# Kernel tuning notes

Hardware: AMD Instinct MI355X
Metric: run time of the kernel (lower is better)

The kernel has to match this reference:

```python
import math
import jax, jax.numpy as jnp
import numpy as np

B, N, D = 16, 2048, 256
EPS = 1e-8  # torch cosine_similarity default eps
TAU = 3.0   # gumbel-softmax temperature


def setup_inputs() -> dict:
    key = jax.random.key(0)
    k1, k2 = jax.random.split(key)
    return {
        "LowLevelFeatures": jax.random.normal(k1, (B, 1, N, D), dtype=jnp.float32),
        "HighLevelFeatures": jax.random.normal(k2, (B, 1, N, D), dtype=jnp.float32),
        "batch_size": B,
    }


def _forward(LLF4, HLF4):
    LLF = LLF4[:, 0]  # [B,N,D]
    HLF = HLF4[:, 0]  # [B,N,D]
    b, n, d = LLF.shape
    # pairwise cosine similarity [B,N,N]: matmul + norm-product (same math as
    # torch's broadcast cosine_similarity, without the [B,N,N,D] intermediate)
    dots = jnp.einsum('bnd,bmd->bnm', LLF, HLF)
    nl = jnp.linalg.norm(LLF, axis=-1)  # [B,N]
    nh = jnp.linalg.norm(HLF, axis=-1)  # [B,N]
    sim = dots / jnp.maximum(nl[:, :, None] * nh[:, None, :], EPS)
    sim = sim / math.sqrt(d)
    probs = jax.nn.softmax(sim, axis=1)  # softmax over dim 1 (LLF rows)
    # F.gumbel_softmax(probs, tau=3, hard=True, dim=1): probs act as logits
    u = jax.random.uniform(jax.random.key(42), probs.shape,
                           minval=1e-10, maxval=1.0)
    gumbels = -jnp.log(-jnp.log(u))
    y_soft = jax.nn.softmax((probs + gumbels) / TAU, axis=1)
    idx = jnp.argmax(y_soft, axis=1)  # [B,N]: selected LLF-row n per HLF col m
    # torch.where on the one-hot scans row-major over (b, n, m), so per batch
    # the returned n-indices are the SORTED multiset of selected indices
    sl = jnp.sort(idx, axis=-1)  # [B,N]
    bidx = jnp.arange(b)[:, None]  # [B,1]
    aligned = HLF[bidx, sl]  # gather along dim 1 -> [B,N,D]
    # rowwise cosine similarity between gathered HLF and LLF
    w = jnp.sum(aligned * LLF, axis=-1) / jnp.maximum(
        jnp.linalg.norm(aligned, axis=-1) * nl, EPS)  # [B,N]
    noise = jax.nn.softmax(w / 0.1, axis=1)[:, :, None]  # [B,N,1]
    hlf_new = aligned + LLF * noise
    out = HLF.at[bidx, sl].set(hlf_new)
    return out


def reference(LowLevelFeatures, HighLevelFeatures, batch_size):
    return _forward(LowLevelFeatures, HighLevelFeatures)
```

## Files before the change

kernel.cpp:

```cpp
#include <hip/hip_runtime.h>
#include <math.h>

#define NB 16
#define NN 2048
#define ND 256
#define BNtot (NB*NN)
#define HH 33554432u

typedef __attribute__((ext_vector_type(8))) short bf16x8;
typedef __attribute__((ext_vector_type(4))) float f32x4;

__device__ __forceinline__ void gld16(const void* g, void* l){
  __builtin_amdgcn_global_load_lds((const __attribute__((address_space(1))) void*)g,
                                   (__attribute__((address_space(3))) void*)l, 16, 0, 0);
}

__device__ __forceinline__ unsigned rotl(unsigned v, int r){
  return __builtin_amdgcn_alignbit(v, v, 32-r);
}
__device__ __forceinline__ unsigned umaxu(unsigned a, unsigned b){ return a > b ? a : b; }
__device__ __forceinline__ unsigned uminu(unsigned a, unsigned b){ return a < b ? a : b; }

__device__ __forceinline__ float gumbelv(unsigned b, unsigned n, unsigned m){
  unsigned f = (b<<22) | (n<<11) | m;
  unsigned x0 = (b < 8u) ? f : (f - HH);
  unsigned x1 = x0 + HH;
  const unsigned ks0=0u, ks1=42u, ks2=0u^42u^0x1BD11BDAu;
  unsigned v0 = x0 + ks0;
  unsigned v1 = x1 + ks1;
#define TFR(r) { v0 += v1; v1 = rotl(v1,(r)); v1 ^= v0; }
  TFR(13) TFR(15) TFR(26) TFR(6)
  v0 += ks1; v1 += ks2 + 1u;
  TFR(17) TFR(29) TFR(16) TFR(24)
  v0 += ks2; v1 += ks0 + 2u;
  TFR(13) TFR(15) TFR(26) TFR(6)
  v0 += ks0; v1 += ks1 + 3u;
  TFR(17) TFR(29) TFR(16) TFR(24)
  v0 += ks1; v1 += ks2 + 4u;
  TFR(13) TFR(15) TFR(26) TFR(6)
  v0 += ks2; v1 += ks0 + 5u;
#undef TFR
  unsigned bits = (b < 8u) ? v0 : v1;
  float fl = __uint_as_float((bits>>9) | 0x3F800000u) - 1.0f;
  float u = fmaxf(1e-10f, fl + 1e-10f);
  return -logf(-logf(u));
}

__device__ __forceinline__ float gfromkey(unsigned key){
  float fl = __uint_as_float(key | 0x3F800000u) - 1.0f;
  float u = fmaxf(1e-10f, fl + 1e-10f);
  return -logf(-logf(u));
}

__global__ void knorms(const float* __restrict__ LLF, const float* __restrict__ HLF,
                       float* __restrict__ nl, float* __restrict__ nh){
  int row = blockIdx.x;
  int wave = threadIdx.x >> 6;
  int lane = threadIdx.x & 63;
  const float* src = wave ? HLF : LLF;
  float4 v = ((const float4*)(src + (size_t)row*ND))[lane];
  float s = v.x*v.x + v.y*v.y + v.z*v.z + v.w*v.w;
  for (int o=32;o;o>>=1) s += __shfl_down(s,o);
  if (lane==0) (wave? nh: nl)[row] = sqrtf(s);
}

__launch_bounds__(256)
__global__ void kprep(const float* __restrict__ LLF, const float* __restrict__ HLF,
                      ushort* __restrict__ Abf, ushort* __restrict__ Bbf,
                      float* __restrict__ nl, float* __restrict__ nh){
  int w    = threadIdx.x >> 6;
  int lane = threadIdx.x & 63;
  int r = blockIdx.x*4 + w;
  const float* src = blockIdx.y ? HLF : LLF;
  ushort* dst      = blockIdx.y ? Bbf : Abf;
  float4 v = ((const float4*)(src + (size_t)r*ND))[lane];
  float s = v.x*v.x + v.y*v.y + v.z*v.z + v.w*v.w;
  for (int o=32;o;o>>=1) s += __shfl_down(s,o);
  if (lane==0) (blockIdx.y ? nh : nl)[r] = sqrtf(s);
  uint2 u;
  u.x = (__float_as_uint(v.y)&0xFFFF0000u)|(__float_as_uint(v.x)>>16);
  u.y = (__float_as_uint(v.w)&0xFFFF0000u)|(__float_as_uint(v.z)>>16);
  int b = r >> 11, nloc = r & 2047;
  int k = lane << 2;
  int ck = k >> 6;
  int j  = k & 63;
  int qi = j >> 3;
  size_t off = (size_t)b*524288 + (size_t)ck*131072 + (size_t)nloc*64
             + ((qi ^ (nloc & 7)) << 3) + (j & 7);
  *(uint2*)(dst + off) = u;
}

#define K1 0.09016844f
__launch_bounds__(256)
__global__ void kgemm_dma(const ushort* __restrict__ Abf, const ushort* __restrict__ Bbf,
                          const float* __restrict__ nl, const float* __restrict__ nh,
                          float* __restrict__ partS){
  __shared__ ushort As[128*64];
  __shared__ ushort Bs[128*64];
  __shared__ float colsum[128];
  const int b  = blockIdx.z;
  const int n0 = blockIdx.y << 7;
  const int m0 = blockIdx.x << 7;
  const int tid  = threadIdx.x;
  const int lane = tid & 63;
  const int w    = tid >> 6;
  const int wn   = w >> 1, wm = w & 1;
  const int quad = lane >> 4, l15 = lane & 15;
  if (tid < 128) colsum[tid] = 0.0f;

  const ushort* Ab = Abf + (size_t)b*524288;
  const ushort* Bb = Bbf + (size_t)b*524288;

  f32x4 acc[4][4];
  #pragma unroll
  for (int i=0;i<4;i++)
    #pragma unroll
    for (int j=0;j<4;j++) acc[i][j] = (f32x4){0.f,0.f,0.f,0.f};

  for (int ck=0; ck<4; ck++){
    __syncthreads();
    const ushort* ga = Ab + (size_t)ck*131072 + (size_t)n0*64;
    const ushort* gb = Bb + (size_t)ck*131072 + (size_t)m0*64;
    #pragma unroll
    for (int t=0;t<4;t++){
      int seg = (w*4 + t) * 512;
      gld16(ga + seg + lane*8, &As[seg]);
      gld16(gb + seg + lane*8, &Bs[seg]);
    }
    __syncthreads();
    #pragma unroll
    for (int ks=0; ks<64; ks+=32){
      bf16x8 af[4], bf[4];
      #pragma unroll
      for (int t=0;t<4;t++){
        int R = wn*64 + t*16 + l15;
        af[t] = *(const bf16x8*)(&As[R*64 + ((((ks>>3)+quad) ^ (R&7))<<3)]);
      }
      #pragma unroll
      for (int t=0;t<4;t++){
        int R = wm*64 + t*16 + l15;
        bf[t] = *(const bf16x8*)(&Bs[R*64 + ((((ks>>3)+quad) ^ (R&7))<<3)]);
      }
      #pragma unroll
      for (int ti=0;ti<4;ti++)
        #pragma unroll
        for (int tj=0;tj<4;tj++)
          acc[ti][tj] = __builtin_amdgcn_mfma_f32_16x16x32_bf16(af[ti], bf[tj], acc[ti][tj], 0, 0, 0);
    }
  }

  float an[4][4];
  #pragma unroll
  for (int ti=0;ti<4;ti++)
    #pragma unroll
    for (int r=0;r<4;r++)
      an[ti][r] = K1 / nl[b*NN + n0 + wn*64 + ti*16 + quad*4 + r];
  float bm[4];
  #pragma unroll
  for (int tj=0;tj<4;tj++)
    bm[tj] = 1.0f / nh[b*NN + m0 + wm*64 + tj*16 + l15];
  #pragma unroll
  for (int tj=0;tj<4;tj++){
    float s = 0.0f;
    #pragma unroll
    for (int ti=0;ti<4;ti++)
      #pragma unroll
      for (int r=0;r<4;r++)
        s += __builtin_amdgcn_exp2f(acc[ti][tj][r]*an[ti][r]*bm[tj] - K1);
    s += __shfl_down(s, 32);
    s += __shfl_down(s, 16);
    if (lane < 16) atomicAdd(&colsum[wm*64 + tj*16 + l15], s);
  }
  __syncthreads();
  if (tid < 128)
    partS[(size_t)blockIdx.y*BNtot + b*NN + m0 + tid] = colsum[tid];
}

__launch_bounds__(256)
__global__ void kgemm_mfma(const float* __restrict__ LLF, const float* __restrict__ HLF,
                           const float* __restrict__ nl, const float* __restrict__ nh,
                           float* __restrict__ partS){
  __shared__ ushort As[128][72];
  __shared__ ushort Bs[128][72];
  __shared__ float colsum[128];
  const int b  = blockIdx.z;
  const int n0 = blockIdx.y << 7;
  const int m0 = blockIdx.x << 7;
  const float* Ab = LLF + (size_t)b*NN*ND;
  const float* Bb = HLF + (size_t)b*NN*ND;
  const int tid  = threadIdx.x;
  const int lane = tid & 63;
  const int w    = tid >> 6;
  const int wn   = w >> 1, wm = w & 1;
  const int quad = lane >> 4, l15 = lane & 15;
  if (tid < 128) colsum[tid] = 0.0f;

  f32x4 acc[4][4];
  #pragma unroll
  for (int i=0;i<4;i++)
    #pragma unroll
    for (int j=0;j<4;j++) acc[i][j] = (f32x4){0.f,0.f,0.f,0.f};

  const int rbase = tid >> 3;
  const int kq    = (tid & 7) << 3;

  for (int ck=0; ck<4; ck++){
    const int k0 = ck << 6;
    __syncthreads();
    #pragma unroll
    for (int pi=0; pi<4; pi++){
      int row = rbase + (pi<<5);
      const float* pa = Ab + (size_t)(n0+row)*ND + k0 + kq;
      float4 a0 = *(const float4*)pa;
      float4 a1 = *(const float4*)(pa+4);
      uint4 ua;
      ua.x = (__float_as_uint(a0.y)&0xFFFF0000u)|(__float_as_uint(a0.x)>>16);
      ua.y = (__float_as_uint(a0.w)&0xFFFF0000u)|(__float_as_uint(a0.z)>>16);
      ua.z = (__float_as_uint(a1.y)&0xFFFF0000u)|(__float_as_uint(a1.x)>>16);
      ua.w = (__float_as_uint(a1.w)&0xFFFF0000u)|(__float_as_uint(a1.z)>>16);
      *(uint4*)(&As[row][kq]) = ua;
      const float* pb = Bb + (size_t)(m0+row)*ND + k0 + kq;
      float4 b0 = *(const float4*)pb;
      float4 b1 = *(const float4*)(pb+4);
      uint4 ub;
      ub.x = (__float_as_uint(b0.y)&0xFFFF0000u)|(__float_as_uint(b0.x)>>16);
      ub.y = (__float_as_uint(b0.w)&0xFFFF0000u)|(__float_as_uint(b0.z)>>16);
      ub.z = (__float_as_uint(b1.y)&0xFFFF0000u)|(__float_as_uint(b1.x)>>16);
      ub.w = (__float_as_uint(b1.w)&0xFFFF0000u)|(__float_as_uint(b1.z)>>16);
      *(uint4*)(&Bs[row][kq]) = ub;
    }
    __syncthreads();
    #pragma unroll
    for (int ks=0; ks<64; ks+=32){
      bf16x8 af[4], bf[4];
      #pragma unroll
      for (int t=0;t<4;t++)
        af[t] = *(const bf16x8*)(&As[wn*64 + t*16 + l15][ks + quad*8]);
      #pragma unroll
      for (int t=0;t<4;t++)
        bf[t] = *(const bf16x8*)(&Bs[wm*64 + t*16 + l15][ks + quad*8]);
      #pragma unroll
      for (int ti=0;ti<4;ti++)
        #pragma unroll
        for (int tj=0;tj<4;tj++)
          acc[ti][tj] = __builtin_amdgcn_mfma_f32_16x16x32_bf16(af[ti], bf[tj], acc[ti][tj], 0, 0, 0);
    }
  }

  float an[4][4];
  #pragma unroll
  for (int ti=0;ti<4;ti++)
    #pragma unroll
    for (int r=0;r<4;r++)
      an[ti][r] = K1 / nl[b*NN + n0 + wn*64 + ti*16 + quad*4 + r];
  float bm[4];
  #pragma unroll
  for (int tj=0;tj<4;tj++)
    bm[tj] = 1.0f / nh[b*NN + m0 + wm*64 + tj*16 + l15];
  #pragma unroll
  for (int tj=0;tj<4;tj++){
    float s = 0.0f;
    #pragma unroll
    for (int ti=0;ti<4;ti++)
      #pragma unroll
      for (int r=0;r<4;r++)
        s += __builtin_amdgcn_exp2f(acc[ti][tj][r]*an[ti][r]*bm[tj] - K1);
    s += __shfl_down(s, 32);
    s += __shfl_down(s, 16);
    if (lane < 16) atomicAdd(&colsum[wm*64 + tj*16 + l15], s);
  }
  __syncthreads();
  if (tid < 128)
    partS[(size_t)blockIdx.y*BNtot + b*NN + m0 + tid] = colsum[tid];
}

__global__ void kScomb(const float* __restrict__ partS, float* __restrict__ iS){
  int g = blockIdx.x*256 + threadIdx.x;
  float s = 0.0f;
  #pragma unroll
  for (int nt=0; nt<16; nt++) s += partS[(size_t)nt*BNtot + g];
  iS[g] = 1.0f/s;
}

__launch_bounds__(256)
__global__ void kgumbel(float* __restrict__ pcv, int* __restrict__ pci){
  int t    = blockIdx.x*256 + threadIdx.x;
  int half = t & 1;
  int m    = (t >> 1) & 2047;
  int bl   = (t >> 12) & 7;
  int nq   = t >> 15;
  int chunkbase = nq << 7;
  int nstart = chunkbase + (half << 6);
  unsigned x0 = ((unsigned)bl << 22) | ((unsigned)nstart << 11) | (unsigned)m;
  const unsigned KS2 = 42u ^ 0x1BD11BDAu;
  unsigned a1=0, a2=0, c1=0, c2=0;
  #pragma unroll 2
  for (int kk = 127 - (half<<6); kk >= 64 - (half<<6); --kk){
    unsigned v0 = x0;
    unsigned v1 = x0 + (HH + 42u);
#define TFR(r) { v0 += v1; v1 = rotl(v1,(r)); v1 ^= v0; }
    TFR(13) TFR(15) TFR(26) TFR(6)
    v0 += 42u;  v1 += KS2 + 1u;
    TFR(17) TFR(29) TFR(16) TFR(24)
    v0 += KS2;  v1 += 2u;
    TFR(13) TFR(15) TFR(26) TFR(6)
     v1 += 42u + 3u;
    TFR(17) TFR(29) TFR(16) TFR(24)
    v0 += 42u;  v1 += KS2 + 4u;
    TFR(13) TFR(15) TFR(26) TFR(6)
    v0 += KS2;  v1 += 5u;
#undef TFR
    unsigned pa = (v0 & 0xFFFFFE00u) | (unsigned)kk;
    unsigned pb = (v1 & 0xFFFFFE00u) | (unsigned)kk;
    unsigned ta = uminu(pa, a1);
    a1 = umaxu(pa, a1);
    a2 = umaxu(ta, a2);
    unsigned tc = uminu(pb, c1);
    c1 = umaxu(pb, c1);
    c2 = umaxu(tc, c2);
    x0 += 2048u;
  }
  unsigned p1 = __shfl_xor((int)a1, 1), p2 = __shfl_xor((int)a2, 1);
  unsigned q1 = __shfl_xor((int)c1, 1), q2 = __shfl_xor((int)c2, 1);
  unsigned A1 = umaxu(a1, p1);
  unsigned A2 = umaxu(uminu(a1, p1), umaxu(a2, p2));
  unsigned C1 = umaxu(c1, q1);
  unsigned C2 = umaxu(uminu(c1, q1), umaxu(c2, q2));
  if (half == 0){
    int baseA = (((nq*NB + bl  )*NN + m) << 1);
    int baseB = (((nq*NB + bl+8)*NN + m) << 1);
    pcv[baseA+0] = gfromkey(A1 >> 9); pci[baseA+0] = chunkbase + 127 - (int)(A1 & 127u);
    pcv[baseA+1] = gfromkey(A2 >> 9); pci[baseA+1] = chunkbase + 127 - (int)(A2 & 127u);
    pcv[baseB+0] = gfromkey(C1 >> 9); pci[baseB+0] = chunkbase + 127 - (int)(C1 & 127u);
    pcv[baseB+1] = gfromkey(C2 >> 9); pci[baseB+1] = chunkbase + 127 - (int)(C2 & 127u);
  }
}

__launch_bounds__(256)
__global__ void kresolve(const float* __restrict__ LLF, const float* __restrict__ HLF,
                         const float* __restrict__ nl, const float* __restrict__ nh,
                         const float* __restrict__ iS,
                         const float* __restrict__ pcv, const int* __restrict__ pci,
                         int* __restrict__ idx){
  int w    = threadIdx.x >> 6;
  int lane = threadIdx.x & 63;
  int g = blockIdx.x*4 + w;
  int b = g >> 11, m = g & 2047;
  float pv = -INFINITY; int pn = 0;
  if (lane < 32){
    int base = ((((lane>>1)*NB + b)*NN + m) << 1) + (lane & 1);
    pv = pcv[base]; pn = pci[base];
  }
  float gmax = pv;
  for (int o=32;o;o>>=1) gmax = fmaxf(gmax, __shfl_down(gmax,o));
  gmax = __shfl(gmax, 0);
  unsigned long long mask = __ballot(pv >= gmax - 8e-5f);
  mask &= 0xFFFFFFFFull;
  float invS = iS[g];
  float bestQ = -INFINITY; int bestN = 1<<30;
  while (mask){
    int src = __builtin_ctzll(mask); mask &= mask-1;
    int   n  = __shfl(pn, src);
    float gv = __shfl(pv, src);
    float4 a = ((const float4*)(LLF + ((size_t)b*NN + n)*ND))[lane];
    float4 h = ((const float4*)(HLF + ((size_t)b*NN + m)*ND))[lane];
    float d = a.x*h.x + a.y*h.y + a.z*h.z + a.w*h.w;
    for (int o=32;o;o>>=1) d += __shfl_down(d,o);
    d = __shfl(d, 0);
    float sim = (d / fmaxf(nl[b*NN+n]*nh[g], 1e-8f)) * 0.0625f;
    float q = expf(sim - 0.0625f)*invS + gv;
    if (q > bestQ || (q == bestQ && n < bestN)){ bestQ = q; bestN = n; }
  }
  if (lane==0) idx[g] = bestN;
}

__launch_bounds__(256)
__global__ void kstats(const float* __restrict__ A, const float* __restrict__ Bm,
                       const float* __restrict__ nl, const float* __restrict__ nh,
                       float* __restrict__ Mout, float* __restrict__ Sinv){
  __shared__ float As[64][33];
  __shared__ float Bs[64][33];
  __shared__ float Cs[64][65];
  const int b  = blockIdx.x >> 5;
  const int m0 = (blockIdx.x & 31) << 6;
  const float* Ab = A  + (size_t)b*NN*ND;
  const float* Bb = Bm + (size_t)b*NN*ND;
  const int tid = threadIdx.x;
  const int tx = tid & 15, ty = tid >> 4;
  float nhv[4];
  #pragma unroll
  for (int j=0;j<4;j++) nhv[j] = nh[b*NN + m0 + tx*4 + j];
  float Mr = -INFINITY, Sr = 0.0f;
  for (int nt=0; nt<NN; nt+=64){
    float acc[4][4] = {{0.f,0.f,0.f,0.f},{0.f,0.f,0.f,0.f},{0.f,0.f,0.f,0.f},{0.f,0.f,0.f,0.f}};
    for (int kc=0; kc<ND; kc+=32){
      __syncthreads();
      #pragma unroll
      for (int s=0;s<2;s++){
        int f = tid + (s<<8);
        int r = f >> 3;
        int c = (f & 7) << 2;
        float4 va = *(const float4*)(Ab + (size_t)(nt+r)*ND + kc + c);
        As[r][c]=va.x; As[r][c+1]=va.y; As[r][c+2]=va.z; As[r][c+3]=va.w;
        float4 vb = *(const float4*)(Bb + (size_t)(m0+r)*ND + kc + c);
        Bs[r][c]=vb.x; Bs[r][c+1]=vb.y; Bs[r][c+2]=vb.z; Bs[r][c+3]=vb.w;
      }
      __syncthreads();
      #pragma unroll 4
      for (int k=0;k<32;k++){
        float a0=As[ty*4+0][k], a1=As[ty*4+1][k], a2=As[ty*4+2][k], a3=As[ty*4+3][k];
        float b0=Bs[tx*4+0][k], b1=Bs[tx*4+1][k], b2=Bs[tx*4+2][k], b3=Bs[tx*4+3][k];
        acc[0][0]+=a0*b0; acc[0][1]+=a0*b1; acc[0][2]+=a0*b2; acc[0][3]+=a0*b3;
        acc[1][0]+=a1*b0; acc[1][1]+=a1*b1; acc[1][2]+=a1*b2; acc[1][3]+=a1*b3;
        acc[2][0]+=a2*b0; acc[2][1]+=a2*b1; acc[2][2]+=a2*b2; acc[2][3]+=a2*b3;
        acc[3][0]+=a3*b0; acc[3][1]+=a3*b1; acc[3][2]+=a3*b2; acc[3][3]+=a3*b3;
      }
    }
    float nlv[4];
    #pragma unroll
    for (int i=0;i<4;i++) nlv[i] = nl[b*NN + nt + ty*4 + i];
    __syncthreads();
    #pragma unroll
    for (int i=0;i<4;i++)
      #pragma unroll
      for (int j=0;j<4;j++){
        float denom = fmaxf(nlv[i]*nhv[j], 1e-8f);
        Cs[ty*4+i][tx*4+j] = (acc[i][j]/denom)*0.0625f;
      }
    __syncthreads();
    if (tid < 64){
      float tmax = -INFINITY;
      #pragma unroll 8
      for (int r=0;r<64;r++) tmax = fmaxf(tmax, Cs[r][tid]);
      float newM = fmaxf(Mr, tmax);
      float s = 0.0f;
      #pragma unroll 4
      for (int r=0;r<64;r++) s += expf(Cs[r][tid]-newM);
      Sr = Sr*expf(Mr-newM) + s;
      Mr = newM;
    }
  }
  if (tid < 64){
    Mout[b*NN+m0+tid] = Mr;
    Sinv[b*NN+m0+tid] = 1.0f/Sr;
  }
}

__launch_bounds__(256)
__global__ void kargmax(const float* __restrict__ A, const float* __restrict__ Bm,
                        const float* __restrict__ nl, const float* __restrict__ nh,
                        const float* __restrict__ Mv, const float* __restrict__ Sv,
                        int* __restrict__ idxout){
  __shared__ float As[64][33];
  __shared__ float Bs[64][33];
  __shared__ float Vs[16][64];
  __shared__ int   Is[16][64];
  const int b  = blockIdx.x >> 5;
  const int m0 = (blockIdx.x & 31) << 6;
  const float* Ab = A  + (size_t)b*NN*ND;
  const float* Bb = Bm + (size_t)b*NN*ND;
  const int tid = threadIdx.x;
  const int tx = tid & 15, ty = tid >> 4;
  float nhv[4], Mj[4], iSj[4];
  #pragma unroll
  for (int j=0;j<4;j++){
    int m = m0 + tx*4 + j;
    nhv[j] = nh[b*NN + m];
    Mj[j]  = Mv[b*NN + m];
    iSj[j] = Sv[b*NN + m];
  }
  float bestV = -INFINITY; int bestN = 0;
  for (int nt=0; nt<NN; nt+=64){
    float acc[4][4] = {{0.f,0.f,0.f,0.f},{0.f,0.f,0.f,0.f},{0.f,0.f,0.f,0.f},{0.f,0.f,0.f,0.f}};
    for (int kc=0; kc<ND; kc+=32){
      __syncthreads();
      #pragma unroll
      for (int s=0;s<2;s++){
        int f = tid + (s<<8);
        int r = f >> 3;
        int c = (f & 7) << 2;
        float4 va = *(const float4*)(Ab + (size_t)(nt+r)*ND + kc + c);
        As[r][c]=va.x; As[r][c+1]=va.y; As[r][c+2]=va.z; As[r][c+3]=va.w;
        float4 vb = *(const float4*)(Bb + (size_t)(m0+r)*ND + kc + c);
        Bs[r][c]=vb.x; Bs[r][c+1]=vb.y; Bs[r][c+2]=vb.z; Bs[r][c+3]=vb.w;
      }
      __syncthreads();
      #pragma unroll 4
      for (int k=0;k<32;k++){
        float a0=As[ty*4+0][k], a1=As[ty*4+1][k], a2=As[ty*4+2][k], a3=As[ty*4+3][k];
        float b0=Bs[tx*4+0][k], b1=Bs[tx*4+1][k], b2=Bs[tx*4+2][k], b3=Bs[tx*4+3][k];
        acc[0][0]+=a0*b0; acc[0][1]+=a0*b1; acc[0][2]+=a0*b2; acc[0][3]+=a0*b3;
        acc[1][0]+=a1*b0; acc[1][1]+=a1*b1; acc[1][2]+=a1*b2; acc[1][3]+=a1*b3;
        acc[2][0]+=a2*b0; acc[2][1]+=a2*b1; acc[2][2]+=a2*b2; acc[2][3]+=a2*b3;
        acc[3][0]+=a3*b0; acc[3][1]+=a3*b1; acc[3][2]+=a3*b2; acc[3][3]+=a3*b3;
      }
    }
    float nlv[4];
    #pragma unroll
    for (int i=0;i<4;i++) nlv[i] = nl[b*NN + nt + ty*4 + i];
    float lv[4]; int li[4];
    #pragma unroll
    for (int j=0;j<4;j++){ lv[j] = -INFINITY; li[j] = 0; }
    #pragma unroll
    for (int i=0;i<4;i++){
      int n = nt + ty*4 + i;
      #pragma unroll
      for (int j=0;j<4;j++){
        float denom = fmaxf(nlv[i]*nhv[j], 1e-8f);
        float sim = (acc[i][j]/denom)*0.0625f;
        float p = expf(sim - Mj[j]) * iSj[j];
        float v = p + gumbelv((unsigned)b, (unsigned)n, (unsigned)(m0 + tx*4 + j));
        if (v > lv[j]) { lv[j] = v; li[j] = n; }
      }
    }
    __syncthreads();
    #pragma unroll
    for (int j=0;j<4;j++){ Vs[ty][tx*4+j]=lv[j]; Is[ty][tx*4+j]=li[j]; }
    __syncthreads();
    if (tid < 64){
      #pragma unroll 4
      for (int t=0;t<16;t++){
        float v = Vs[t][tid];
        if (v > bestV){ bestV = v; bestN = Is[t][tid]; }
      }
    }
  }
  if (tid < 64) idxout[b*NN + m0 + tid] = bestN;
}

__global__ void ksort(const int* __restrict__ idx, int* __restrict__ cntg,
                      int* __restrict__ offg, int* __restrict__ sl){
  __shared__ int c[NN];
  __shared__ int part[256];
  int b = blockIdx.x, tid = threadIdx.x;
  for (int v=tid; v<NN; v+=256) c[v]=0;
  __syncthreads();
  for (int j=tid; j<NN; j+=256) atomicAdd(&c[idx[b*NN+j]], 1);
  __syncthreads();
  int base = tid*8, s=0, lc[8];
  #pragma unroll
  for (int k=0;k<8;k++){ lc[k]=c[base+k]; s+=lc[k]; }
  part[tid]=s; __syncthreads();
  for (int o=1;o<256;o<<=1){
    int v = (tid>=o)? part[tid-o] : 0;
    __syncthreads();
    part[tid]+=v;
    __syncthreads();
  }
  int run = part[tid]-s;
  #pragma unroll
  for (int k=0;k<8;k++){
    int v = base+k;
    cntg[b*NN+v]=lc[k];
    offg[b*NN+v]=run;
    for (int j=0;j<lc[k];j++) sl[b*NN+run+j]=v;
    run += lc[k];
  }
}

__global__ void kw(const float* __restrict__ LLF, const float* __restrict__ HLF,
                   const float* __restrict__ nl, const float* __restrict__ nh,
                   const int* __restrict__ sl, float* __restrict__ w){
  int g = blockIdx.x*4 + (threadIdx.x>>6);
  int lane = threadIdx.x & 63;
  int b = g >> 11;
  int s = sl[g];
  float4 a = ((const float4*)(HLF + ((size_t)b*NN + s)*ND))[lane];
  float4 l = ((const float4*)(LLF + (size_t)g*ND))[lane];
  float d = a.x*l.x + a.y*l.y + a.z*l.z + a.w*l.w;
  for (int o=32;o;o>>=1) d += __shfl_down(d,o);
  if (lane==0){
    float denom = fmaxf(nh[b*NN+s]*nl[g], 1e-8f);
    w[g] = d/denom;
  }
}

__global__ void knoise(const float* __restrict__ w, float* __restrict__ nz){
  int b = blockIdx.x, tid = threadIdx.x;
  __shared__ float sred[4];
  float x[8]; float mx = -INFINITY;
  #pragma unroll
  for (int k=0;k<8;k++){ x[k] = w[b*NN + tid*8 + k] / 0.1f; mx = fmaxf(mx, x[k]); }
  for (int o=32;o;o>>=1) mx = fmaxf(mx, __shfl_down(mx,o));
  mx = __shfl(mx, 0);
  if ((tid&63)==0) sred[tid>>6] = mx;
  __syncthreads();
  mx = fmaxf(fmaxf(sred[0],sred[1]), fmaxf(sred[2],sred[3]));
  __syncthreads();
  float e[8]; float s = 0.f;
  #pragma unroll
  for (int k=0;k<8;k++){ e[k] = expf(x[k]-mx); s += e[k]; }
  for (int o=32;o;o>>=1) s += __shfl_down(s,o);
  s = __shfl(s, 0);
  if ((tid&63)==0) sred[tid>>6] = s;
  __syncthreads();
  s = sred[0]+sred[1]+sred[2]+sred[3];
  #pragma unroll
  for (int k=0;k<8;k++) nz[b*NN + tid*8 + k] = e[k]/s;
}

__global__ void kfinal(const float* __restrict__ LLF, const float* __restrict__ HLF,
                       const int* __restrict__ cnt, const int* __restrict__ off,
                       const float* __restrict__ nz, float* __restrict__ out){
  int row = blockIdx.x;
  int lane = threadIdx.x;
  int b = row >> 11;
  float4 h = ((const float4*)(HLF + (size_t)row*ND))[lane];
  int c = cnt[row];
  if (c > 0){
    int i = off[row] + c - 1;
    float ns = nz[b*NN + i];
    float4 l = ((const float4*)(LLF + ((size_t)(b*NN + i))*ND))[lane];
    h.x += l.x*ns; h.y += l.y*ns; h.z += l.z*ns; h.w += l.w*ns;
  }
  ((float4*)(out + (size_t)row*ND))[lane] = h;
}

extern "C" void kernel_launch(void* const* d_in, const int* in_sizes, int n_in,
                              void* d_out, int out_size, void* d_ws, size_t ws_size,
                              hipStream_t stream){
  const float* LLF = (const float*)d_in[0];
  const float* HLF = (const float*)d_in[1];
  float* out = (float*)d_out;
  float* ws = (float*)d_ws;

  float* nl  = ws;
  float* nh  = ws + 1*(size_t)BNtot;
  float* iS  = ws + 2*(size_t)BNtot;
  int*   idx = (int*)(ws + 3*(size_t)BNtot);
  int*   cnt = (int*)(ws + 4*(size_t)BNtot);
  int*   off = (int*)(ws + 5*(size_t)BNtot);
  int*   sl  = (int*)(ws + 6*(size_t)BNtot);
  float* wv  = ws + 7*(size_t)BNtot;
  float* nz  = ws + 8*(size_t)BNtot;
  float* partS = ws + 9*(size_t)BNtot;
  float* pcv   = partS + 16*(size_t)BNtot;
  int*   pci   = (int*)(pcv + 32*(size_t)BNtot);
  ushort* Abf  = (ushort*)(pci + 32*(size_t)BNtot);
  ushort* Bbf  = Abf + (size_t)BNtot*ND;
  const size_t needBytes1 = (9 + 16 + 32 + 32) * (size_t)BNtot * 4;
  const size_t needBytes2 = needBytes1 + 2 * (size_t)BNtot * ND * 2;

  if (ws_size >= needBytes2){
    hipLaunchKernelGGL(kprep,    dim3(BNtot/4, 2), dim3(256), 0, stream, LLF, HLF, Abf, Bbf, nl, nh);
    hipLaunchKernelGGL(kgemm_dma,dim3(16,16,16),   dim3(256), 0, stream, Abf, Bbf, nl, nh, partS);
    hipLaunchKernelGGL(kScomb,   dim3(BNtot/256),  dim3(256), 0, stream, partS, iS);
    hipLaunchKernelGGL(kgumbel,  dim3(2048),       dim3(256), 0, stream, pcv, pci);
    hipLaunchKernelGGL(kresolve, dim3(BNtot/4),    dim3(256), 0, stream, LLF, HLF, nl, nh, iS, pcv, pci, idx);
  } else if (ws_size >= needBytes1){
    hipLaunchKernelGGL(knorms,   dim3(BNtot),      dim3(128), 0, stream, LLF, HLF, nl, nh);
    hipLaunchKernelGGL(kgemm_mfma,dim3(16,16,16),  dim3(256), 0, stream, LLF, HLF, nl, nh, partS);
    hipLaunchKernelGGL(kScomb,   dim3(BNtot/256),  dim3(256), 0, stream, partS, iS);
    hipLaunchKernelGGL(kgumbel,  dim3(2048),       dim3(256), 0, stream, pcv, pci);
    hipLaunchKernelGGL(kresolve, dim3(BNtot/4),    dim3(256), 0, stream, LLF, HLF, nl, nh, iS, pcv, pci, idx);
  } else {
    float* Mv = ws + 9*(size_t)BNtot;
    hipLaunchKernelGGL(knorms,   dim3(BNtot),      dim3(128), 0, stream, LLF, HLF, nl, nh);
    hipLaunchKernelGGL(kstats,   dim3(NB*32),      dim3(256), 0, stream, LLF, HLF, nl, nh, Mv, iS);
    hipLaunchKernelGGL(kargmax,  dim3(NB*32),      dim3(256), 0, stream, LLF, HLF, nl, nh, Mv, iS, idx);
  }

  hipLaunchKernelGGL(ksort,  dim3(NB),      dim3(256), 0, stream, idx, cnt, off, sl);
  hipLaunchKernelGGL(kw,     dim3(BNtot/4), dim3(256), 0, stream, LLF, HLF, nl, nh, sl, wv);
  hipLaunchKernelGGL(knoise, dim3(NB),      dim3(256), 0, stream, wv, nz);
  hipLaunchKernelGGL(kfinal, dim3(BNtot),   dim3(64),  0, stream, LLF, HLF, cnt, off, nz, out);
}
```

Before: 304.5 us.

## Co-schedule gumbel blocks inside prep and GEMM kernels, fold Scomb into resolve

The standalone gumbel-noise kernel's 2048 blocks are split across the prep kernel (768 blocks) and the GEMM kernel (5 of every 21 blocks), so the ALU-heavy Threefry hashing runs alongside the memory-bound prep and the MFMA GEMM. The partial column-sum combine kernel is removed, and kresolve now reduces the 16 partials itself with a shuffle. The resolve loop also hoists the HLF row and norm loads, and the hash loop uses a small round-injection rewrite with unroll 4. This cuts two launches and overlaps independent work. The risk is that GEMM blocks see uneven scheduling and lower occupancy from the mixed block types.

```diff
diff --git a/kernel.cpp b/kernel.cpp
--- a/kernel.cpp
+++ b/kernel.cpp
@@ -6,6 +6,9 @@
 #define ND 256
 #define BNtot (NB*NN)
 #define HH 33554432u
+
+#define GF1 768
+#define GF2 1280
 
 typedef __attribute__((ext_vector_type(8))) short bf16x8;
 typedef __attribute__((ext_vector_type(4))) float f32x4;
@@ -52,6 +55,68 @@
   return -logf(-logf(u));
 }
 
+__device__ __forceinline__ void gumbel_body(int gb, float* __restrict__ pcv, int* __restrict__ pci){
+  int t    = gb*256 + (int)threadIdx.x;
+  int half = t & 1;
+  int m    = (t >> 1) & 2047;
+  int bl   = (t >> 12) & 7;
+  int nq   = t >> 15;
+  int chunkbase = nq << 7;
+  int nstart = chunkbase + (half << 6);
+  unsigned x0 = ((unsigned)bl << 22) | ((unsigned)nstart << 11) | (unsigned)m;
+  const unsigned KS2 = 42u ^ 0x1BD11BDAu;
+  unsigned a1=0, a2=0, c1=0, c2=0;
+  unsigned vk = (unsigned)(127 - (half<<6));
+#define TFR(r)       { v0 += v1; v1 = rotl(v1,(r)); v1 ^= v0; }
+#define TFRI(r, inj) { v0 += v1 + (inj); v1 = rotl(v1,(r)); v1 ^= v0; }
+  #pragma unroll 4
+  for (int j = 0; j < 64; ++j){
+    unsigned v0 = x0;
+    unsigned v1 = x0 + (HH + 42u);
+    TFR(13) TFR(15) TFR(26) TFR(6)
+    v1 += KS2 + 1u;
+    TFRI(17, 42u) TFR(29) TFR(16) TFR(24)
+    v1 += 2u;
+    TFRI(13, KS2) TFR(15) TFR(26) TFR(6)
+    v1 += 42u + 3u;
+    TFR(17) TFR(29) TFR(16) TFR(24)
+    v1 += KS2 + 4u;
+    TFRI(13, 42u) TFR(15) TFR(26) TFR(6)
+    v0 += KS2; v1 += 5u;
+    unsigned pa = (v0 & 0xFFFFFE00u) | vk;
+    unsigned pb = (v1 & 0xFFFFFE00u) | vk;
+    unsigned ta = uminu(pa, a1);
+    a1 = umaxu(pa, a1);
+    a2 = umaxu(ta, a2);
+    unsigned tc = uminu(pb, c1);
+    c1 = umaxu(pb, c1);
+    c2 = umaxu(tc, c2);
+    x0 += 2048u;
+    vk -= 1u;
+  }
+#undef TFR
+#undef TFRI
+  unsigned p1 = __shfl_xor((int)a1, 1), p2 = __shfl_xor((int)a2, 1);
+  unsigned q1 = __shfl_xor((int)c1, 1), q2 = __shfl_xor((int)c2, 1);
+  unsigned A1 = umaxu(a1, p1);
+  unsigned A2 = umaxu(uminu(a1, p1), umaxu(a2, p2));
+  unsigned C1 = umaxu(c1, q1);
+  unsigned C2 = umaxu(uminu(c1, q1), umaxu(c2, q2));
+  if (half == 0){
+    int baseA = (((nq*NB + bl  )*NN + m) << 1);
+    int baseB = (((nq*NB + bl+8)*NN + m) << 1);
+    pcv[baseA+0] = gfromkey(A1 >> 9); pci[baseA+0] = chunkbase + 127 - (int)(A1 & 127u);
+    pcv[baseA+1] = gfromkey(A2 >> 9); pci[baseA+1] = chunkbase + 127 - (int)(A2 & 127u);
+    pcv[baseB+0] = gfromkey(C1 >> 9); pci[baseB+0] = chunkbase + 127 - (int)(C1 & 127u);
+    pcv[baseB+1] = gfromkey(C2 >> 9); pci[baseB+1] = chunkbase + 127 - (int)(C2 & 127u);
+  }
+}
+
+__launch_bounds__(256)
+__global__ void kgumbel(float* __restrict__ pcv, int* __restrict__ pci){
+  gumbel_body(blockIdx.x, pcv, pci);
+}
+
 __global__ void knorms(const float* __restrict__ LLF, const float* __restrict__ HLF,
                        float* __restrict__ nl, float* __restrict__ nh){
   int row = blockIdx.x;
@@ -65,18 +130,24 @@
 }
 
 __launch_bounds__(256)
-__global__ void kprep(const float* __restrict__ LLF, const float* __restrict__ HLF,
-                      ushort* __restrict__ Abf, ushort* __restrict__ Bbf,
-                      float* __restrict__ nl, float* __restrict__ nh){
+__global__ void kfuse1(const float* __restrict__ LLF, const float* __restrict__ HLF,
+                       ushort* __restrict__ Abf, ushort* __restrict__ Bbf,
+                       float* __restrict__ nl, float* __restrict__ nh,
+                       float* __restrict__ pcv, int* __restrict__ pci){
+  int bid = blockIdx.x;
+  if (bid < GF1){ gumbel_body(GF2 + bid, pcv, pci); return; }
+  int pid = bid - GF1;
+  int px  = pid & 8191;
+  int py  = pid >> 13;
   int w    = threadIdx.x >> 6;
   int lane = threadIdx.x & 63;
-  int r = blockIdx.x*4 + w;
-  const float* src = blockIdx.y ? HLF : LLF;
-  ushort* dst      = blockIdx.y ? Bbf : Abf;
+  int r = px*4 + w;
+  const float* src = py ? HLF : LLF;
+  ushort* dst      = py ? Bbf : Abf;
   float4 v = ((const float4*)(src + (size_t)r*ND))[lane];
   float s = v.x*v.x + v.y*v.y + v.z*v.z + v.w*v.w;
   for (int o=32;o;o>>=1) s += __shfl_down(s,o);
-  if (lane==0) (blockIdx.y ? nh : nl)[r] = sqrtf(s);
+  if (lane==0) (py ? nh : nl)[r] = sqrtf(s);
   uint2 u;
   u.x = (__float_as_uint(v.y)&0xFFFF0000u)|(__float_as_uint(v.x)>>16);
   u.y = (__float_as_uint(v.w)&0xFFFF0000u)|(__float_as_uint(v.z)>>16);
@@ -92,15 +163,20 @@
 
 #define K1 0.09016844f
 __launch_bounds__(256)
-__global__ void kgemm_dma(const ushort* __restrict__ Abf, const ushort* __restrict__ Bbf,
-                          const float* __restrict__ nl, const float* __restrict__ nh,
-                          float* __restrict__ partS){
+__global__ void kfuse2(const ushort* __restrict__ Abf, const ushort* __restrict__ Bbf,
+                       const float* __restrict__ nl, const float* __restrict__ nh,
+                       float* __restrict__ partS,
+                       float* __restrict__ pcv, int* __restrict__ pci){
   __shared__ ushort As[128*64];
   __shared__ ushort Bs[128*64];
   __shared__ float colsum[128];
-  const int b  = blockIdx.z;
-  const int n0 = blockIdx.y << 7;
-  const int m0 = blockIdx.x << 7;
+  int bid = blockIdx.x;
+  int grp = bid / 21, rr = bid % 21;
+  if (rr < 5){ gumbel_body(grp*5 + rr, pcv, pci); return; }
+  int g  = grp*16 + (rr - 5);
+  const int b  = g >> 8;
+  const int n0 = ((g >> 4) & 15) << 7;
+  const int m0 = (g & 15) << 7;
   const int tid  = threadIdx.x;
   const int lane = tid & 63;
   const int w    = tid >> 6;
@@ -173,7 +249,7 @@
   }
   __syncthreads();
   if (tid < 128)
-    partS[(size_t)blockIdx.y*BNtot + b*NN + m0 + tid] = colsum[tid];
+    partS[(size_t)((g >> 4) & 15)*BNtot + b*NN + m0 + tid] = colsum[tid];
 }
 
 __launch_bounds__(256)
@@ -274,78 +350,22 @@
     partS[(size_t)blockIdx.y*BNtot + b*NN + m0 + tid] = colsum[tid];
 }
 
-__global__ void kScomb(const float* __restrict__ partS, float* __restrict__ iS){
-  int g = blockIdx.x*256 + threadIdx.x;
-  float s = 0.0f;
-  #pragma unroll
-  for (int nt=0; nt<16; nt++) s += partS[(size_t)nt*BNtot + g];
-  iS[g] = 1.0f/s;
-}
-
-__launch_bounds__(256)
-__global__ void kgumbel(float* __restrict__ pcv, int* __restrict__ pci){
-  int t    = blockIdx.x*256 + threadIdx.x;
-  int half = t & 1;
-  int m    = (t >> 1) & 2047;
-  int bl   = (t >> 12) & 7;
-  int nq   = t >> 15;
-  int chunkbase = nq << 7;
-  int nstart = chunkbase + (half << 6);
-  unsigned x0 = ((unsigned)bl << 22) | ((unsigned)nstart << 11) | (unsigned)m;
-  const unsigned KS2 = 42u ^ 0x1BD11BDAu;
-  unsigned a1=0, a2=0, c1=0, c2=0;
-  #pragma unroll 2
-  for (int kk = 127 - (half<<6); kk >= 64 - (half<<6); --kk){
-    unsigned v0 = x0;
-    unsigned v1 = x0 + (HH + 42u);
-#define TFR(r) { v0 += v1; v1 = rotl(v1,(r)); v1 ^= v0; }
-    TFR(13) TFR(15) TFR(26) TFR(6)
-    v0 += 42u;  v1 += KS2 + 1u;
-    TFR(17) TFR(29) TFR(16) TFR(24)
-    v0 += KS2;  v1 += 2u;
-    TFR(13) TFR(15) TFR(26) TFR(6)
-     v1 += 42u + 3u;
-    TFR(17) TFR(29) TFR(16) TFR(24)
-    v0 += 42u;  v1 += KS2 + 4u;
-    TFR(13) TFR(15) TFR(26) TFR(6)
-    v0 += KS2;  v1 += 5u;
-#undef TFR
-    unsigned pa = (v0 & 0xFFFFFE00u) | (unsigned)kk;
-    unsigned pb = (v1 & 0xFFFFFE00u) | (unsigned)kk;
-    unsigned ta = uminu(pa, a1);
-    a1 = umaxu(pa, a1);
-    a2 = umaxu(ta, a2);
-    unsigned tc = uminu(pb, c1);
-    c1 = umaxu(pb, c1);
-    c2 = umaxu(tc, c2);
-    x0 += 2048u;
-  }
-  unsigned p1 = __shfl_xor((int)a1, 1), p2 = __shfl_xor((int)a2, 1);
-  unsigned q1 = __shfl_xor((int)c1, 1), q2 = __shfl_xor((int)c2, 1);
-  unsigned A1 = umaxu(a1, p1);
-  unsigned A2 = umaxu(uminu(a1, p1), umaxu(a2, p2));
-  unsigned C1 = umaxu(c1, q1);
-  unsigned C2 = umaxu(uminu(c1, q1), umaxu(c2, q2));
-  if (half == 0){
-    int baseA = (((nq*NB + bl  )*NN + m) << 1);
-    int baseB = (((nq*NB + bl+8)*NN + m) << 1);
-    pcv[baseA+0] = gfromkey(A1 >> 9); pci[baseA+0] = chunkbase + 127 - (int)(A1 & 127u);
-    pcv[baseA+1] = gfromkey(A2 >> 9); pci[baseA+1] = chunkbase + 127 - (int)(A2 & 127u);
-    pcv[baseB+0] = gfromkey(C1 >> 9); pci[baseB+0] = chunkbase + 127 - (int)(C1 & 127u);
-    pcv[baseB+1] = gfromkey(C2 >> 9); pci[baseB+1] = chunkbase + 127 - (int)(C2 & 127u);
-  }
-}
-
 __launch_bounds__(256)
 __global__ void kresolve(const float* __restrict__ LLF, const float* __restrict__ HLF,
                          const float* __restrict__ nl, const float* __restrict__ nh,
-                         const float* __restrict__ iS,
+                         const float* __restrict__ partS,
                          const float* __restrict__ pcv, const int* __restrict__ pci,
                          int* __restrict__ idx){
   int w    = threadIdx.x >> 6;
   int lane = threadIdx.x & 63;
   int g = blockIdx.x*4 + w;
   int b = g >> 11, m = g & 2047;
+  float ps = (lane < 16) ? partS[(size_t)lane*BNtot + g] : 0.0f;
+  ps += __shfl_down(ps, 8);
+  ps += __shfl_down(ps, 4);
+  ps += __shfl_down(ps, 2);
+  ps += __shfl_down(ps, 1);
+  float invS = 1.0f / __shfl(ps, 0);
   float pv = -INFINITY; int pn = 0;
   if (lane < 32){
     int base = ((((lane>>1)*NB + b)*NN + m) << 1) + (lane & 1);
@@ -356,18 +376,18 @@
   gmax = __shfl(gmax, 0);
   unsigned long long mask = __ballot(pv >= gmax - 8e-5f);
   mask &= 0xFFFFFFFFull;
-  float invS = iS[g];
+  float4 h = ((const float4*)(HLF + (size_t)g*ND))[lane];
+  float nhg = nh[g];
   float bestQ = -INFINITY; int bestN = 1<<30;
   while (mask){
     int src = __builtin_ctzll(mask); mask &= mask-1;
     int   n  = __shfl(pn, src);
     float gv = __shfl(pv, src);
     float4 a = ((const float4*)(LLF + ((size_t)b*NN + n)*ND))[lane];
-    float4 h = ((const float4*)(HLF + ((size_t)b*NN + m)*ND))[lane];
     float d = a.x*h.x + a.y*h.y + a.z*h.z + a.w*h.w;
     for (int o=32;o;o>>=1) d += __shfl_down(d,o);
     d = __shfl(d, 0);
-    float sim = (d / fmaxf(nl[b*NN+n]*nh[g], 1e-8f)) * 0.0625f;
+    float sim = (d / fmaxf(nl[b*NN+n]*nhg, 1e-8f)) * 0.0625f;
     float q = expf(sim - 0.0625f)*invS + gv;
     if (q > bestQ || (q == bestQ && n < bestN)){ bestQ = q; bestN = n; }
   }
@@ -642,17 +662,14 @@
   const size_t needBytes2 = needBytes1 + 2 * (size_t)BNtot * ND * 2;
 
   if (ws_size >= needBytes2){
-    hipLaunchKernelGGL(kprep,    dim3(BNtot/4, 2), dim3(256), 0, stream, LLF, HLF, Abf, Bbf, nl, nh);
-    hipLaunchKernelGGL(kgemm_dma,dim3(16,16,16),   dim3(256), 0, stream, Abf, Bbf, nl, nh, partS);
-    hipLaunchKernelGGL(kScomb,   dim3(BNtot/256),  dim3(256), 0, stream, partS, iS);
-    hipLaunchKernelGGL(kgumbel,  dim3(2048),       dim3(256), 0, stream, pcv, pci);
-    hipLaunchKernelGGL(kresolve, dim3(BNtot/4),    dim3(256), 0, stream, LLF, HLF, nl, nh, iS, pcv, pci, idx);
+    hipLaunchKernelGGL(kfuse1,  dim3(GF1 + 16384), dim3(256), 0, stream, LLF, HLF, Abf, Bbf, nl, nh, pcv, pci);
+    hipLaunchKernelGGL(kfuse2,  dim3(21*256),      dim3(256), 0, stream, Abf, Bbf, nl, nh, partS, pcv, pci);
+    hipLaunchKernelGGL(kresolve,dim3(BNtot/4),     dim3(256), 0, stream, LLF, HLF, nl, nh, partS, pcv, pci, idx);
   } else if (ws_size >= needBytes1){
     hipLaunchKernelGGL(knorms,   dim3(BNtot),      dim3(128), 0, stream, LLF, HLF, nl, nh);
     hipLaunchKernelGGL(kgemm_mfma,dim3(16,16,16),  dim3(256), 0, stream, LLF, HLF, nl, nh, partS);
-    hipLaunchKernelGGL(kScomb,   dim3(BNtot/256),  dim3(256), 0, stream, partS, iS);
     hipLaunchKernelGGL(kgumbel,  dim3(2048),       dim3(256), 0, stream, pcv, pci);
-    hipLaunchKernelGGL(kresolve, dim3(BNtot/4),    dim3(256), 0, stream, LLF, HLF, nl, nh, iS, pcv, pci, idx);
+    hipLaunchKernelGGL(kresolve, dim3(BNtot/4),    dim3(256), 0, stream, LLF, HLF, nl, nh, partS, pcv, pci, idx);
   } else {
     float* Mv = ws + 9*(size_t)BNtot;
     hipLaunchKernelGGL(knorms,   dim3(BNtot),      dim3(128), 0, stream, LLF, HLF, nl, nh);
```

Result: no change. 302.0 us (-0.8%).
